# Performance work log

Measured on AMD Instinct MI355X. Metric: run time of the kernel, lower is better.

## Reference

```python
import jax, jax.numpy as jnp
import numpy as np

DIM = 192
NUM_HEADS = 6
WINDOW = (2, 6, 12)
INPUT_RES = (8, 48, 180)
TYPE_OF_WINDOWS = (INPUT_RES[0] // WINDOW[0]) * (INPUT_RES[1] // WINDOW[1])  # 32
N_TOK = WINDOW[0] * WINDOW[1] * WINDOW[2]  # 144
NLON = INPUT_RES[2] // WINDOW[2]  # 15
TABLE_ROWS = WINDOW[0] ** 2 * WINDOW[1] ** 2 * (2 * WINDOW[2] - 1)  # 3312


def calculate_position_bias_indices(ws):
    wz, wh, ww = ws
    zi = np.arange(wz)
    zj = -np.arange(wz) * wz
    hi = np.arange(wh)
    hj = -np.arange(wh) * wh
    w = np.arange(ww)
    c1 = np.stack(np.meshgrid(zi, hi, w, indexing='ij')).reshape(3, -1)
    c2 = np.stack(np.meshgrid(zj, hj, w, indexing='ij')).reshape(3, -1)
    coords = (c1[:, :, None] - c2[:, None, :]).transpose(1, 2, 0).copy()
    coords[:, :, 2] += ww - 1
    coords[:, :, 1] *= 2 * ww - 1
    coords[:, :, 0] *= (2 * ww - 1) * wh * wh
    return coords.sum(-1)  # (N, N) in [0, TABLE_ROWS)


def setup_inputs() -> dict:
    key = jax.random.key(0)
    ks = jax.random.split(key, 7)
    B_ = NLON  # batch=1 times nLon window columns
    x = jax.random.normal(ks[0], (B_, TYPE_OF_WINDOWS, N_TOK, DIM), dtype=jnp.float32)
    mask = jax.random.normal(ks[1], (NLON, TYPE_OF_WINDOWS, N_TOK, N_TOK), dtype=jnp.float32)
    qkv_w = jax.random.normal(ks[2], (3 * DIM, DIM), dtype=jnp.float32) * 0.02
    qkv_b = jax.random.normal(ks[3], (3 * DIM,), dtype=jnp.float32) * 0.02
    proj_w = jax.random.normal(ks[4], (DIM, DIM), dtype=jnp.float32) * 0.02
    proj_b = jax.random.normal(ks[5], (DIM,), dtype=jnp.float32) * 0.02
    bias_table = jax.random.normal(ks[6], (TABLE_ROWS, TYPE_OF_WINDOWS, NUM_HEADS), dtype=jnp.float32) * 0.02
    position_index = jnp.asarray(calculate_position_bias_indices(WINDOW), dtype=jnp.int64)
    return {"x": x, "mask": mask, "qkv_w": qkv_w, "qkv_b": qkv_b,
            "proj_w": proj_w, "proj_b": proj_b, "bias_table": bias_table,
            "position_index": position_index}


def reference(x, mask, qkv_w, qkv_b, proj_w, proj_b, bias_table, position_index):
    B_, nW_, N, C = x.shape
    H = NUM_HEADS
    hd = C // H
    scale = hd ** (-0.5)
    # qkv projection: (B_, nW_, N, 3, H, hd)
    qkv = (jnp.einsum('bwnc,dc->bwnd', x, qkv_w) + qkv_b).reshape(B_, nW_, N, 3, H, hd)
    q = qkv[:, :, :, 0] * scale  # (B_, nW_, N, H, hd)
    k = qkv[:, :, :, 1]
    v = qkv[:, :, :, 2]
    # attention scores: (B_, H, nW_, N, N)
    attn = jnp.einsum('bwihd,bwjhd->bhwij', q, k)
    # gathered earth position bias -> (H, nW_, N, N)
    bias = bias_table[position_index.reshape(-1)]  # (N*N, nW_, H)
    bias = bias.reshape(N, N, nW_, H).transpose(3, 2, 0, 1)
    attn = attn + bias[None]
    # mask add: view (B_//nLon, nLon, H, nW_, N, N) + mask (nLon, 1, nW_, N, N)
    nLon = mask.shape[0]
    attn = attn.reshape(B_ // nLon, nLon, H, nW_, N, N) + mask[None, :, None]
    attn = attn.reshape(B_, H, nW_, N, N)
    attn = jax.nn.softmax(attn, axis=-1)
    out = jnp.einsum('bhwij,bwjhd->bwihd', attn, v).reshape(B_, nW_, N, C)
    out = jnp.einsum('bwnc,dc->bwnd', out, proj_w) + proj_b
    return out
```

## Files before the change

kernel.cpp:

```cpp
#include <hip/hip_runtime.h>
#include <hip/hip_bf16.h>

#define B_LON 15
#define NW    32
#define NTOK  144
#define DIM   192
#define NH    6
#define HD    32
#define K3    576
#define MROWS (B_LON*NW*NTOK)
#define NN    (NTOK*NTOK)
#define SCALE 0.17677669529663687f

typedef __attribute__((ext_vector_type(8))) short bf16x8;
typedef __attribute__((ext_vector_type(8))) unsigned short u16x8;
typedef __attribute__((ext_vector_type(4))) float f32x4;

__device__ inline unsigned short f2bf(float f) {
  __bf16 h = (__bf16)f;
  return __builtin_bit_cast(unsigned short, h);
}
__device__ inline float bf2f(unsigned short u) {
  union { unsigned int i; float f; } c;
  c.i = ((unsigned int)u) << 16;
  return c.f;
}

#define NX8 1658880
#define NQ8 13824
#define NP8 4608

__global__ __launch_bounds__(256) void conv_bf_k(
    const float* __restrict__ x, const float* __restrict__ qw,
    const float* __restrict__ pw,
    unsigned short* __restrict__ xbf, unsigned short* __restrict__ qwbf,
    unsigned short* __restrict__ pwbf) {
  const long gid = (long)blockIdx.x * 256 + threadIdx.x;
  const float* src;
  unsigned short* dst;
  long off;
  if (gid < NX8)            { src = x;  dst = xbf;  off = gid; }
  else if (gid < NX8 + NQ8) { src = qw; dst = qwbf; off = gid - NX8; }
  else                      { src = pw; dst = pwbf; off = gid - NX8 - NQ8; }
  const float4 a = ((const float4*)src)[off * 2];
  const float4 b = ((const float4*)src)[off * 2 + 1];
  u16x8 u = {f2bf(a.x), f2bf(a.y), f2bf(a.z), f2bf(a.w),
             f2bf(b.x), f2bf(b.y), f2bf(b.z), f2bf(b.w)};
  *(u16x8*)&dst[off * 8] = u;
}

__global__ __launch_bounds__(256) void bias_pre_k(
    const float* __restrict__ btab, const int* __restrict__ pos,
    unsigned short* __restrict__ biasb) {
  const int wh  = blockIdx.x;
  const int seg = blockIdx.y * 2304;
  unsigned short* dst = biasb + (size_t)wh * NN;
#pragma unroll
  for (int it = 0; it < 9; ++it) {
    const int e = seg + it * 256 + threadIdx.x;
    dst[e] = f2bf(btab[(size_t)pos[e] * (NW * NH) + wh]);
  }
}

__global__ __launch_bounds__(192, 3) void fused_attn_k(
    const unsigned short* __restrict__ X, const unsigned short* __restrict__ W,
    const float* __restrict__ Bv, const float* __restrict__ mask,
    const unsigned short* __restrict__ biasb, unsigned short* __restrict__ ao) {
  __shared__ unsigned short Qs[NTOK * 36];
  __shared__ unsigned short Ks[NTOK * 36];
  __shared__ unsigned short Vs[32 * 160];
  __shared__ unsigned short Ps[3 * 16 * 168];

  const int t    = threadIdx.x;
  const int wave = t / 64;
  const int lane = t & 63;
  const int ln15 = lane & 15;
  const int quad = lane >> 4;
  const int idx  = blockIdx.x;
  const int h    = idx / 480;
  const int bw   = idx % 480;
  const int w    = bw & 31;
  const int wh   = w * NH + h;
  const float* maskp = mask + (size_t)bw * NN;
  const unsigned short* biasp = biasb + (size_t)wh * NN;
  unsigned short* ps = &Ps[wave * 16 * 168];
  const int wv3 = wave * 3;

  if (t < 64) {
    u16x8 z = {0, 0, 0, 0, 0, 0, 0, 0};
    *(u16x8*)&Vs[(t >> 1) * 160 + 144 + (t & 1) * 8] = z;
  }
  {
    ushort4 z = {0, 0, 0, 0};
    *(ushort4*)&ps[(lane >> 2) * 168 + 144 + (lane & 3) * 4] = z;
  }

  f32x4 acc[3][6];
#pragma unroll
  for (int mt = 0; mt < 3; ++mt)
#pragma unroll
    for (int nt = 0; nt < 6; ++nt) acc[mt][nt] = (f32x4){0.f, 0.f, 0.f, 0.f};

#pragma unroll
  for (int kk = 0; kk < 6; ++kk) {
    const int k0 = kk * 32 + quad * 8;
    bf16x8 af[3], bfr[6];
#pragma unroll
    for (int mt = 0; mt < 3; ++mt)
      af[mt] = *(const bf16x8*)&X[(size_t)(bw * NTOK + (wv3 + mt) * 16 + ln15) * DIM + k0];
#pragma unroll
    for (int nt = 0; nt < 6; ++nt) {
      const int wrow = (nt >> 1) * DIM + h * HD + (nt & 1) * 16 + ln15;
      bfr[nt] = *(const bf16x8*)&W[(size_t)wrow * DIM + k0];
    }
#pragma unroll
    for (int mt = 0; mt < 3; ++mt)
#pragma unroll
      for (int nt = 0; nt < 6; ++nt)
        acc[mt][nt] = __builtin_amdgcn_mfma_f32_16x16x32_bf16(
            af[mt], bfr[nt], acc[mt][nt], 0, 0, 0);
  }

#pragma unroll
  for (int nt = 0; nt < 6; ++nt) {
    const int dd   = (nt & 1) * 16 + ln15;
    const float bias = Bv[(nt >> 1) * DIM + h * HD + dd];
#pragma unroll
    for (int mt = 0; mt < 3; ++mt) {
      const int tok = (wv3 + mt) * 16 + quad * 4;
#pragma unroll
      for (int r = 0; r < 4; ++r) {
        const float v = acc[mt][nt][r] + bias;
        if (nt < 2)      Qs[(tok + r) * 36 + dd] = f2bf(v * SCALE);
        else if (nt < 4) Ks[(tok + r) * 36 + dd] = f2bf(v);
        else             Vs[dd * 160 + tok + r]  = f2bf(v);
      }
    }
  }
  __syncthreads();

  for (int g = wv3; g < wv3 + 3; ++g) {
    const int i0 = g * 16;
    const int ib = i0 + quad * 4;

    const bf16x8 qf = *(const bf16x8*)&Qs[(i0 + ln15) * 36 + quad * 8];
    f32x4 s[9];
#pragma unroll
    for (int jt = 0; jt < 9; ++jt) {
      const bf16x8 kf = *(const bf16x8*)&Ks[(jt * 16 + ln15) * 36 + quad * 8];
      s[jt] = (f32x4){0.f, 0.f, 0.f, 0.f};
      s[jt] = __builtin_amdgcn_mfma_f32_16x16x32_bf16(qf, kf, s[jt], 0, 0, 0);
    }

#pragma unroll
    for (int jt = 0; jt < 9; ++jt) {
      const int j = jt * 16 + ln15;
#pragma unroll
      for (int r = 0; r < 4; ++r) {
        const int ij = (ib + r) * NTOK + j;
        s[jt][r] += bf2f(biasp[ij]) + maskp[ij];
      }
    }

    float rinv[4];
#pragma unroll
    for (int r = 0; r < 4; ++r) {
      float mx = s[0][r];
#pragma unroll
      for (int jt = 1; jt < 9; ++jt) mx = fmaxf(mx, s[jt][r]);
#pragma unroll
      for (int off = 1; off < 16; off <<= 1) mx = fmaxf(mx, __shfl_xor(mx, off));
      float sum = 0.f;
#pragma unroll
      for (int jt = 0; jt < 9; ++jt) {
        const float e = __expf(s[jt][r] - mx);
        s[jt][r] = e;
        sum += e;
      }
#pragma unroll
      for (int off = 1; off < 16; off <<= 1) sum += __shfl_xor(sum, off);
      rinv[r] = 1.0f / sum;
    }

#pragma unroll
    for (int jt = 0; jt < 9; ++jt)
#pragma unroll
      for (int r = 0; r < 4; ++r)
        ps[(quad * 4 + r) * 168 + jt * 16 + ln15] = f2bf(s[jt][r]);

    f32x4 o[2] = {{0.f, 0.f, 0.f, 0.f}, {0.f, 0.f, 0.f, 0.f}};
#pragma unroll
    for (int kt = 0; kt < 5; ++kt) {
      const bf16x8 pf = *(const bf16x8*)&ps[ln15 * 168 + kt * 32 + quad * 8];
#pragma unroll
      for (int nt = 0; nt < 2; ++nt) {
        const bf16x8 vf = *(const bf16x8*)&Vs[(nt * 16 + ln15) * 160 + kt * 32 + quad * 8];
        o[nt] = __builtin_amdgcn_mfma_f32_16x16x32_bf16(pf, vf, o[nt], 0, 0, 0);
      }
    }

#pragma unroll
    for (int nt = 0; nt < 2; ++nt)
#pragma unroll
      for (int r = 0; r < 4; ++r)
        ao[(size_t)(bw * NTOK + ib + r) * DIM + h * HD + nt * 16 + ln15] =
            f2bf(o[nt][r] * rinv[r]);
  }
}

__global__ __launch_bounds__(256) void proj_gemm_k(
    const unsigned short* __restrict__ AO, const unsigned short* __restrict__ W,
    const float* __restrict__ Bv, float* __restrict__ out) {
  __shared__ unsigned short As[64 * 200];
  __shared__ unsigned short Bs[64 * 200];
  const int t    = threadIdx.x;
  const int n0   = blockIdx.x * 64;
  const int m0   = blockIdx.y * 64;
  const int w    = t >> 6;
  const int lane = t & 63;
  const int ln15 = lane & 15;
  const int quad = lane >> 4;

#pragma unroll
  for (int it = t; it < 1536; it += 256) {
    const int row = it / 24;
    const int c8  = (it % 24) * 8;
    *(u16x8*)&As[row * 200 + c8] = *(const u16x8*)&AO[(size_t)(m0 + row) * 192 + c8];
  }
#pragma unroll
  for (int it = t; it < 1536; it += 256) {
    const int row = it / 24;
    const int c8  = (it % 24) * 8;
    *(u16x8*)&Bs[row * 200 + c8] = *(const u16x8*)&W[(size_t)(n0 + row) * 192 + c8];
  }
  __syncthreads();

  f32x4 acc[4];
#pragma unroll
  for (int j = 0; j < 4; ++j) acc[j] = (f32x4){0.f, 0.f, 0.f, 0.f};

#pragma unroll
  for (int k0 = 0; k0 < 192; k0 += 32) {
    const bf16x8 af = *(bf16x8*)&As[(w * 16 + ln15) * 200 + k0 + quad * 8];
#pragma unroll
    for (int nt = 0; nt < 4; ++nt) {
      const bf16x8 bfr = *(bf16x8*)&Bs[(nt * 16 + ln15) * 200 + k0 + quad * 8];
      acc[nt] = __builtin_amdgcn_mfma_f32_16x16x32_bf16(af, bfr, acc[nt], 0, 0, 0);
    }
  }

#pragma unroll
  for (int nt = 0; nt < 4; ++nt) {
    const int colg = n0 + nt * 16 + ln15;
    const float bias = Bv[colg];
#pragma unroll
    for (int r = 0; r < 4; ++r) {
      const int m = m0 + w * 16 + quad * 4 + r;
      out[(size_t)m * 192 + colg] = acc[nt][r] + bias;
    }
  }
}

extern "C" void kernel_launch(void* const* d_in, const int* in_sizes, int n_in,
                              void* d_out, int out_size, void* d_ws, size_t ws_size,
                              hipStream_t stream) {
  const float* x      = (const float*)d_in[0];
  const float* mask   = (const float*)d_in[1];
  const float* qkv_w  = (const float*)d_in[2];
  const float* qkv_b  = (const float*)d_in[3];
  const float* proj_w = (const float*)d_in[4];
  const float* proj_b = (const float*)d_in[5];
  const float* btab   = (const float*)d_in[6];
  const int*   pos    = (const int*)d_in[7];
  float* out = (float*)d_out;

  unsigned short* ws = (unsigned short*)d_ws;
  const size_t sz = (size_t)MROWS * DIM;
  unsigned short* aobuf = ws;
  unsigned short* biasb = ws + sz + 256;
  unsigned short* xbf   = biasb + (size_t)192 * NN + 256;
  unsigned short* qwbf  = xbf + sz;
  unsigned short* pwbf  = qwbf + (size_t)K3 * DIM;

  conv_bf_k<<<NX8 / 256 + NQ8 / 256 + NP8 / 256, 256, 0, stream>>>(
      x, qkv_w, proj_w, xbf, qwbf, pwbf);
  bias_pre_k<<<dim3(NW * NH, 9), 256, 0, stream>>>(btab, pos, biasb);
  fused_attn_k<<<NH * 480, 192, 0, stream>>>(
      xbf, qwbf, qkv_b, mask, biasb, aobuf);
  proj_gemm_k<<<dim3(DIM / 64, MROWS / 64), 256, 0, stream>>>(
      aobuf, pwbf, proj_b, out);
}
```

Before: 290.8 us.

## Widen attention blocks to 9 waves, stage bias column in LDS, reshape proj GEMM

The fused attention kernel now launches 576 threads per block, so each of 9 waves handles one 16-row tile instead of 3 waves handling 3 tiles each. This aims at more latency hiding and fewer registers per thread, at the cost of a larger LDS P buffer. Block indices are also remapped so blocks sharing a window column land on the same XCD, which should improve L2 reuse of mask and x. The bias precompute first gathers the per-(window,head) table column into shared memory so strided global reads are not repeated per element. The projection GEMM drops LDS staging and computes all 192 output columns per block straight from global memory.

After: 386.2 us. 32.8% more time.

```diff
diff --git a/kernel.cpp b/kernel.cpp
--- a/kernel.cpp
+++ b/kernel.cpp
@@ -10,6 +10,7 @@
 #define K3    576
 #define MROWS (B_LON*NW*NTOK)
 #define NN    (NTOK*NTOK)
+#define TROWS 3312
 #define SCALE 0.17677669529663687f
 
 typedef __attribute__((ext_vector_type(8))) short bf16x8;
@@ -52,24 +53,29 @@
 __global__ __launch_bounds__(256) void bias_pre_k(
     const float* __restrict__ btab, const int* __restrict__ pos,
     unsigned short* __restrict__ biasb) {
-  const int wh  = blockIdx.x;
-  const int seg = blockIdx.y * 2304;
+  __shared__ float col[TROWS];
+  const int wh = blockIdx.x;
+  const int t  = threadIdx.x;
+  for (int i = t; i < TROWS; i += 256)
+    col[i] = btab[(size_t)i * (NW * NH) + wh];
+  __syncthreads();
   unsigned short* dst = biasb + (size_t)wh * NN;
-#pragma unroll
-  for (int it = 0; it < 9; ++it) {
-    const int e = seg + it * 256 + threadIdx.x;
-    dst[e] = f2bf(btab[(size_t)pos[e] * (NW * NH) + wh]);
-  }
-}
-
-__global__ __launch_bounds__(192, 3) void fused_attn_k(
+  const int seg = blockIdx.y * 6912;
+#pragma unroll
+  for (int it = 0; it < 27; ++it) {
+    const int e = seg + it * 256 + t;
+    dst[e] = f2bf(col[pos[e]]);
+  }
+}
+
+__global__ __launch_bounds__(576, 5) void fused_attn_k(
     const unsigned short* __restrict__ X, const unsigned short* __restrict__ W,
     const float* __restrict__ Bv, const float* __restrict__ mask,
     const unsigned short* __restrict__ biasb, unsigned short* __restrict__ ao) {
   __shared__ unsigned short Qs[NTOK * 36];
   __shared__ unsigned short Ks[NTOK * 36];
   __shared__ unsigned short Vs[32 * 160];
-  __shared__ unsigned short Ps[3 * 16 * 168];
+  __shared__ unsigned short Ps[9 * 16 * 168];
 
   const int t    = threadIdx.x;
   const int wave = t / 64;
@@ -77,14 +83,15 @@
   const int ln15 = lane & 15;
   const int quad = lane >> 4;
   const int idx  = blockIdx.x;
-  const int h    = idx / 480;
-  const int bw   = idx % 480;
+  const int xcd  = idx & 7;
+  const int j0   = idx >> 3;
+  const int h    = j0 % 6;
+  const int bw   = (j0 / 6) * 8 + xcd;
   const int w    = bw & 31;
   const int wh   = w * NH + h;
   const float* maskp = mask + (size_t)bw * NN;
   const unsigned short* biasp = biasb + (size_t)wh * NN;
   unsigned short* ps = &Ps[wave * 16 * 168];
-  const int wv3 = wave * 3;
 
   if (t < 64) {
     u16x8 z = {0, 0, 0, 0, 0, 0, 0, 0};
@@ -95,52 +102,43 @@
     *(ushort4*)&ps[(lane >> 2) * 168 + 144 + (lane & 3) * 4] = z;
   }
 
-  f32x4 acc[3][6];
-#pragma unroll
-  for (int mt = 0; mt < 3; ++mt)
-#pragma unroll
-    for (int nt = 0; nt < 6; ++nt) acc[mt][nt] = (f32x4){0.f, 0.f, 0.f, 0.f};
+  f32x4 acc[6];
+#pragma unroll
+  for (int nt = 0; nt < 6; ++nt) acc[nt] = (f32x4){0.f, 0.f, 0.f, 0.f};
 
 #pragma unroll
   for (int kk = 0; kk < 6; ++kk) {
     const int k0 = kk * 32 + quad * 8;
-    bf16x8 af[3], bfr[6];
-#pragma unroll
-    for (int mt = 0; mt < 3; ++mt)
-      af[mt] = *(const bf16x8*)&X[(size_t)(bw * NTOK + (wv3 + mt) * 16 + ln15) * DIM + k0];
+    const bf16x8 af =
+        *(const bf16x8*)&X[(size_t)(bw * NTOK + wave * 16 + ln15) * DIM + k0];
+    bf16x8 bfr[6];
 #pragma unroll
     for (int nt = 0; nt < 6; ++nt) {
       const int wrow = (nt >> 1) * DIM + h * HD + (nt & 1) * 16 + ln15;
       bfr[nt] = *(const bf16x8*)&W[(size_t)wrow * DIM + k0];
     }
 #pragma unroll
-    for (int mt = 0; mt < 3; ++mt)
-#pragma unroll
-      for (int nt = 0; nt < 6; ++nt)
-        acc[mt][nt] = __builtin_amdgcn_mfma_f32_16x16x32_bf16(
-            af[mt], bfr[nt], acc[mt][nt], 0, 0, 0);
+    for (int nt = 0; nt < 6; ++nt)
+      acc[nt] = __builtin_amdgcn_mfma_f32_16x16x32_bf16(af, bfr[nt], acc[nt], 0, 0, 0);
   }
 
 #pragma unroll
   for (int nt = 0; nt < 6; ++nt) {
     const int dd   = (nt & 1) * 16 + ln15;
     const float bias = Bv[(nt >> 1) * DIM + h * HD + dd];
-#pragma unroll
-    for (int mt = 0; mt < 3; ++mt) {
-      const int tok = (wv3 + mt) * 16 + quad * 4;
-#pragma unroll
-      for (int r = 0; r < 4; ++r) {
-        const float v = acc[mt][nt][r] + bias;
-        if (nt < 2)      Qs[(tok + r) * 36 + dd] = f2bf(v * SCALE);
-        else if (nt < 4) Ks[(tok + r) * 36 + dd] = f2bf(v);
-        else             Vs[dd * 160 + tok + r]  = f2bf(v);
-      }
+    const int tok = wave * 16 + quad * 4;
+#pragma unroll
+    for (int r = 0; r < 4; ++r) {
+      const float v = acc[nt][r] + bias;
+      if (nt < 2)      Qs[(tok + r) * 36 + dd] = f2bf(v * SCALE);
+      else if (nt < 4) Ks[(tok + r) * 36 + dd] = f2bf(v);
+      else             Vs[dd * 160 + tok + r]  = f2bf(v);
     }
   }
   __syncthreads();
 
-  for (int g = wv3; g < wv3 + 3; ++g) {
-    const int i0 = g * 16;
+  {
+    const int i0 = wave * 16;
     const int ib = i0 + quad * 4;
 
     const bf16x8 qf = *(const bf16x8*)&Qs[(i0 + ln15) * 36 + quad * 8];
@@ -208,56 +206,42 @@
   }
 }
 
-__global__ __launch_bounds__(256) void proj_gemm_k(
+__global__ __launch_bounds__(256, 4) void proj_gemm_k(
     const unsigned short* __restrict__ AO, const unsigned short* __restrict__ W,
     const float* __restrict__ Bv, float* __restrict__ out) {
-  __shared__ unsigned short As[64 * 200];
-  __shared__ unsigned short Bs[64 * 200];
   const int t    = threadIdx.x;
-  const int n0   = blockIdx.x * 64;
-  const int m0   = blockIdx.y * 64;
   const int w    = t >> 6;
   const int lane = t & 63;
   const int ln15 = lane & 15;
   const int quad = lane >> 4;
-
-#pragma unroll
-  for (int it = t; it < 1536; it += 256) {
-    const int row = it / 24;
-    const int c8  = (it % 24) * 8;
-    *(u16x8*)&As[row * 200 + c8] = *(const u16x8*)&AO[(size_t)(m0 + row) * 192 + c8];
-  }
-#pragma unroll
-  for (int it = t; it < 1536; it += 256) {
-    const int row = it / 24;
-    const int c8  = (it % 24) * 8;
-    *(u16x8*)&Bs[row * 200 + c8] = *(const u16x8*)&W[(size_t)(n0 + row) * 192 + c8];
-  }
-  __syncthreads();
-
-  f32x4 acc[4];
-#pragma unroll
-  for (int j = 0; j < 4; ++j) acc[j] = (f32x4){0.f, 0.f, 0.f, 0.f};
-
-#pragma unroll
-  for (int k0 = 0; k0 < 192; k0 += 32) {
-    const bf16x8 af = *(bf16x8*)&As[(w * 16 + ln15) * 200 + k0 + quad * 8];
-#pragma unroll
-    for (int nt = 0; nt < 4; ++nt) {
-      const bf16x8 bfr = *(bf16x8*)&Bs[(nt * 16 + ln15) * 200 + k0 + quad * 8];
-      acc[nt] = __builtin_amdgcn_mfma_f32_16x16x32_bf16(af, bfr, acc[nt], 0, 0, 0);
-    }
-  }
-
-#pragma unroll
-  for (int nt = 0; nt < 4; ++nt) {
-    const int colg = n0 + nt * 16 + ln15;
+  const int m0   = blockIdx.x * 64;
+  const int mrow = m0 + w * 16 + ln15;
+
+  f32x4 acc[12];
+#pragma unroll
+  for (int nt = 0; nt < 12; ++nt) acc[nt] = (f32x4){0.f, 0.f, 0.f, 0.f};
+
+#pragma unroll
+  for (int kk = 0; kk < 6; ++kk) {
+    const int k0 = kk * 32 + quad * 8;
+    const bf16x8 af = *(const bf16x8*)&AO[(size_t)mrow * DIM + k0];
+    bf16x8 bfr[12];
+#pragma unroll
+    for (int nt = 0; nt < 12; ++nt)
+      bfr[nt] = *(const bf16x8*)&W[(size_t)(nt * 16 + ln15) * DIM + k0];
+#pragma unroll
+    for (int nt = 0; nt < 12; ++nt)
+      acc[nt] = __builtin_amdgcn_mfma_f32_16x16x32_bf16(af, bfr[nt], acc[nt], 0, 0, 0);
+  }
+
+#pragma unroll
+  for (int nt = 0; nt < 12; ++nt) {
+    const int colg = nt * 16 + ln15;
     const float bias = Bv[colg];
-#pragma unroll
-    for (int r = 0; r < 4; ++r) {
-      const int m = m0 + w * 16 + quad * 4 + r;
-      out[(size_t)m * 192 + colg] = acc[nt][r] + bias;
-    }
+    const int mbase = m0 + w * 16 + quad * 4;
+#pragma unroll
+    for (int r = 0; r < 4; ++r)
+      out[(size_t)(mbase + r) * DIM + colg] = acc[nt][r] + bias;
   }
 }
 
@@ -284,9 +268,9 @@
 
   conv_bf_k<<<NX8 / 256 + NQ8 / 256 + NP8 / 256, 256, 0, stream>>>(
       x, qkv_w, proj_w, xbf, qwbf, pwbf);
-  bias_pre_k<<<dim3(NW * NH, 9), 256, 0, stream>>>(btab, pos, biasb);
-  fused_attn_k<<<NH * 480, 192, 0, stream>>>(
+  bias_pre_k<<<dim3(NW * NH, 3), 256, 0, stream>>>(btab, pos, biasb);
+  fused_attn_k<<<NH * 480, 576, 0, stream>>>(
       xbf, qwbf, qkv_b, mask, biasb, aobuf);
-  proj_gemm_k<<<dim3(DIM / 64, MROWS / 64), 256, 0, stream>>>(
+  proj_gemm_k<<<MROWS / 64, 256, 0, stream>>>(
       aobuf, pwbf, proj_b, out);
 }
```
